# Performance work log

Measured on AMD Instinct MI355X. Metric: run time of the kernel, lower is better.

Reference implementation:

```python
import jax, jax.numpy as jnp
import numpy as np

QUERY_DIM = 1024
CONTEXT_DIM = 1024
HEADS = 8
DIM_HEAD = 64
INNER = HEADS * DIM_HEAD  # 512
SCALE = DIM_HEAD ** -0.5


def setup_inputs() -> dict:
    key = jax.random.key(0)
    ks = jax.random.split(key, 7)
    B, N, M = 2, 2048, 2048
    x = jax.random.normal(ks[0], (B, N, QUERY_DIM), dtype=jnp.float32)
    context = jax.random.normal(ks[1], (B, M, CONTEXT_DIM), dtype=jnp.float32)
    # nn.Linear weights (stored as [out, in] in torch; we use [in, out] here)
    Wq = jax.random.normal(ks[2], (QUERY_DIM, INNER), dtype=jnp.float32) * (QUERY_DIM ** -0.5)
    Wk = jax.random.normal(ks[3], (CONTEXT_DIM, INNER), dtype=jnp.float32) * (CONTEXT_DIM ** -0.5)
    Wv = jax.random.normal(ks[4], (CONTEXT_DIM, INNER), dtype=jnp.float32) * (CONTEXT_DIM ** -0.5)
    Wo = jax.random.normal(ks[5], (INNER, QUERY_DIM), dtype=jnp.float32) * (INNER ** -0.5)
    bo = jax.random.normal(ks[6], (QUERY_DIM,), dtype=jnp.float32) * 0.01
    return {"x": x, "context": context, "Wq": Wq, "Wk": Wk, "Wv": Wv, "Wo": Wo, "bo": bo}


def reference(x, context, Wq, Wk, Wv, Wo, bo):
    B, N, _ = x.shape
    M = context.shape[1]
    # projections (no bias, matching nn.Linear(bias=False))
    q = (x @ Wq).reshape(B, N, HEADS, DIM_HEAD)          # b i h d
    k = (context @ Wk).reshape(B, M, HEADS, DIM_HEAD)    # b j h d
    v = (context @ Wv).reshape(B, M, HEADS, DIM_HEAD)    # b j h d
    # scores in fp32 (ATTN_PRECISION=='fp32' path)
    sim = jnp.einsum('bihd,bjhd->bhij', q.astype(jnp.float32), k.astype(jnp.float32)) * SCALE
    attn = jax.nn.softmax(sim, axis=-1).astype(v.dtype)  # b h i j
    out = jnp.einsum('bhij,bjhd->bihd', attn, v).reshape(B, N, INNER)
    return out @ Wo + bo  # dropout p=0.0 is identity
```

## Files before the change

### kernel.cpp

```cpp
#include <hip/hip_runtime.h>
#include <math.h>

typedef __bf16 bf16_t;
typedef __bf16 bf16x8 __attribute__((ext_vector_type(8)));
typedef __bf16 bf16x4 __attribute__((ext_vector_type(4)));
typedef float  f32x4  __attribute__((ext_vector_type(4)));

#define MFMA16(a, b, c) __builtin_amdgcn_mfma_f32_16x16x32_bf16((a), (b), (c), 0, 0, 0)

#define INNER   512
#define DHEAD   64
#define QSCALE  0.18033688f

__device__ __forceinline__ void g2l(const bf16_t* g, bf16_t* l) {
  __builtin_amdgcn_global_load_lds(
      (const __attribute__((address_space(1))) unsigned int*)g,
      (__attribute__((address_space(3))) unsigned int*)l, 16, 0, 0);
}

__global__ __launch_bounds__(256) void pre_k(const float* __restrict__ x,
                                             const float* __restrict__ ctx,
                                             const float* __restrict__ Wq,
                                             const float* __restrict__ Wk,
                                             const float* __restrict__ Wv,
                                             const float* __restrict__ Wo,
                                             bf16_t* __restrict__ xb,
                                             bf16_t* __restrict__ cb,
                                             bf16_t* __restrict__ WqT,
                                             bf16_t* __restrict__ WkT,
                                             bf16_t* __restrict__ WvT,
                                             bf16_t* __restrict__ WoT) {
  __shared__ float tile[64][65];
  int bx = blockIdx.x;
  if (bx < 8192) {
    const float* in = (bx >= 4096) ? ctx : x;
    bf16_t* out     = (bx >= 4096) ? cb  : xb;
    int i = (bx & 4095) * 256 + threadIdx.x;
    float4 f = ((const float4*)in)[i];
    bf16x4 v = { (bf16_t)f.x, (bf16_t)f.y, (bf16_t)f.z, (bf16_t)f.w };
    ((bf16x4*)out)[i] = v;
    return;
  }
  int t = bx - 8192;
  int z = t >> 7, bid = t & 127;
  const float* W; bf16_t* WT; int K, N;
  if (z == 0)      { W = Wq; WT = WqT; K = 1024; N = 512; }
  else if (z == 1) { W = Wk; WT = WkT; K = 1024; N = 512; }
  else if (z == 2) { W = Wv; WT = WvT; K = 1024; N = 512; }
  else             { W = Wo; WT = WoT; K = 512;  N = 1024; }
  int tK = K >> 6;
  int kt = bid % tK, nt = bid / tK;
  int k0 = kt << 6, n0 = nt << 6;
  for (int idx = threadIdx.x; idx < 4096; idx += 256) {
    int r = idx >> 6, c = idx & 63;
    tile[r][c] = W[(size_t)(k0 + r) * N + n0 + c];
  }
  __syncthreads();
  for (int idx = threadIdx.x; idx < 4096; idx += 256) {
    int r = idx >> 6, c = idx & 63;
    WT[(size_t)(n0 + r) * K + k0 + c] = (bf16_t)tile[c][r];
  }
}

__device__ __forceinline__ void gemm128(const bf16_t* __restrict__ A,
                                        const bf16_t* __restrict__ Bt,
                                        int K, int N, int row0, int n0,
                                        int mode, float scale,
                                        bf16_t* __restrict__ Cb,
                                        float* __restrict__ Cf,
                                        const float* __restrict__ bias) {
  __shared__ bf16_t As[2 * 128 * 64];
  __shared__ bf16_t Bs[2 * 128 * 64];
  const int tid = threadIdx.x;
  const int w = tid >> 6, lane = tid & 63, quad = lane >> 4, l16 = lane & 15;

  const int sr8  = lane >> 3;
  const int slog = ((lane & 7) ^ sr8) << 3;
  const bf16_t* ga = A  + (size_t)(row0 + w * 32 + sr8) * K + slog;
  const bf16_t* gb = Bt + (size_t)(n0   + w * 32 + sr8) * K + slog;
  bf16_t* lA = As + w * 2048;
  bf16_t* lB = Bs + w * 2048;

  f32x4 acc[4][4];
#pragma unroll
  for (int i = 0; i < 4; ++i)
#pragma unroll
    for (int j = 0; j < 4; ++j) acc[i][j] = f32x4{0.f, 0.f, 0.f, 0.f};

  const int mrow = (w & 1) << 6, ncol = (w >> 1) << 6;
  const int KT = K >> 6;

#pragma unroll
  for (int p = 0; p < 4; ++p) {
    g2l(ga + (size_t)(p * 8) * K, lA + p * 512);
    g2l(gb + (size_t)(p * 8) * K, lB + p * 512);
  }

  for (int kc = 0; kc < KT; ++kc) {
    const int cur = (kc & 1) * 8192, nxt = ((kc + 1) & 1) * 8192;
    __syncthreads();
    if (kc + 1 < KT) {
      const int k0 = (kc + 1) * 64;
#pragma unroll
      for (int p = 0; p < 4; ++p) {
        g2l(ga + (size_t)(p * 8) * K + k0, lA + nxt + p * 512);
        g2l(gb + (size_t)(p * 8) * K + k0, lB + nxt + p * 512);
      }
    }
#pragma unroll
    for (int ks = 0; ks < 2; ++ks) {
      const int phys = ((ks * 4 + quad) ^ (l16 & 7)) << 3;
      bf16x8 af[4], bfr[4];
#pragma unroll
      for (int i = 0; i < 4; ++i)
        af[i] = *(const bf16x8*)&As[cur + (mrow + i * 16 + l16) * 64 + phys];
#pragma unroll
      for (int j = 0; j < 4; ++j)
        bfr[j] = *(const bf16x8*)&Bs[cur + (ncol + j * 16 + l16) * 64 + phys];
#pragma unroll
      for (int i = 0; i < 4; ++i)
#pragma unroll
        for (int j = 0; j < 4; ++j)
          acc[i][j] = MFMA16(af[i], bfr[j], acc[i][j]);
    }
  }

#pragma unroll
  for (int i = 0; i < 4; ++i) {
    int row = row0 + mrow + i * 16 + quad * 4;
#pragma unroll
    for (int j = 0; j < 4; ++j) {
      int col = n0 + ncol + j * 16 + l16;
      if (mode == 2) {
        int bb = row >> 11, key = row & 2047;
        int hh = col >> 6,  d   = col & 63;
        bf16x4 v = { (bf16_t)acc[i][j][0], (bf16_t)acc[i][j][1],
                     (bf16_t)acc[i][j][2], (bf16_t)acc[i][j][3] };
        *(bf16x4*)&Cb[((size_t)((bb * 8 + hh) * 64 + d)) * 2048 + key] = v;
      } else {
#pragma unroll
        for (int r = 0; r < 4; ++r) {
          if (mode == 1) Cf[(size_t)(row + r) * N + col] = acc[i][j][r] + bias[col];
          else           Cb[(size_t)(row + r) * N + col] = (bf16_t)(acc[i][j][r] * scale);
        }
      }
    }
  }
}

__global__ __launch_bounds__(256, 2) void gemm_qkv_k(const bf16_t* __restrict__ xb,
                                                     const bf16_t* __restrict__ cb,
                                                     const bf16_t* __restrict__ WqT,
                                                     const bf16_t* __restrict__ WkT,
                                                     const bf16_t* __restrict__ WvT,
                                                     bf16_t* __restrict__ Qb,
                                                     bf16_t* __restrict__ Kb,
                                                     bf16_t* __restrict__ Vt) {
  int z = blockIdx.z;
  const bf16_t* A  = (z == 0) ? xb  : cb;
  const bf16_t* Bt = (z == 0) ? WqT : (z == 1) ? WkT : WvT;
  bf16_t* C        = (z == 0) ? Qb  : (z == 1) ? Kb  : Vt;
  int mode         = (z == 2) ? 2 : 0;
  float scale      = (z == 0) ? QSCALE : 1.0f;
  gemm128(A, Bt, 1024, 512, blockIdx.y * 128, blockIdx.x * 128, mode, scale,
          C, nullptr, nullptr);
}

__global__ __launch_bounds__(256, 2) void gemm_out_k(const bf16_t* __restrict__ AO,
                                                     const bf16_t* __restrict__ WoT,
                                                     const float* __restrict__ bo,
                                                     float* __restrict__ out) {
  gemm128(AO, WoT, 512, 1024, blockIdx.y * 128, blockIdx.x * 128, 1, 1.0f,
          nullptr, out, bo);
}

__global__ __launch_bounds__(256, 2) void attn_k(const bf16_t* __restrict__ Qb,
                                                 const bf16_t* __restrict__ Kb,
                                                 const bf16_t* __restrict__ Vt,
                                                 bf16_t* __restrict__ AO) {
  const int tid = threadIdx.x;
  const int w = tid >> 6, lane = tid & 63, quad = lane >> 4, l16 = lane & 15;
  const int qt = blockIdx.x;
  const int bh = blockIdx.y;
  const int b = bh >> 3, h = bh & 7;

  __shared__ bf16_t Ks[2 * 128 * 64];
  __shared__ bf16_t Vs[64 * 128];
  __shared__ bf16_t Ps[64 * 136];

  const int qrow = b * 2048 + qt * 64 + w * 16 + l16;
  const bf16_t* qptr = Qb + (size_t)qrow * INNER + h * DHEAD;
  bf16x8 bq[2];
  bq[0] = *(const bf16x8*)(qptr + quad * 8);
  bq[1] = *(const bf16x8*)(qptr + 32 + quad * 8);

  f32x4 o[4];
#pragma unroll
  for (int dt = 0; dt < 4; ++dt) o[dt] = f32x4{0.f, 0.f, 0.f, 0.f};
  float m_s = -__builtin_inff(), l_s = 0.f;

  const bf16_t* kbase  = Kb + ((size_t)b * 2048) * INNER + h * DHEAD;
  const bf16_t* vtbase = Vt + ((size_t)bh * 64) * 2048;

  const int krow = lane >> 3;
  const int kcol = ((lane & 7) ^ (lane >> 3)) << 3;
  const int vrow = lane >> 4;

#pragma unroll
  for (int p = 0; p < 4; ++p)
    g2l(kbase + (size_t)(w * 32 + p * 8 + krow) * INNER + kcol,
        &Ks[w * 2048 + p * 512]);

  for (int kt = 0; kt < 16; ++kt) {
    const int cur = (kt & 1) * 8192, nxt = ((kt + 1) & 1) * 8192;
    __syncthreads();
    if (kt < 16 - 1) {
#pragma unroll
      for (int p = 0; p < 4; ++p)
        g2l(kbase + (size_t)((kt + 1) * 128 + w * 32 + p * 8 + krow) * INNER + kcol,
            &Ks[nxt + w * 2048 + p * 512]);
    }
#pragma unroll
    for (int p = 0; p < 4; ++p) {
      int vlog = ((lane & 15) ^ ((p * 4 + vrow) & 15)) << 3;
      g2l(vtbase + (size_t)(w * 16 + p * 4 + vrow) * 2048 + kt * 128 + vlog,
          &Vs[w * 2048 + p * 512]);
    }

    f32x4 s[8];
#pragma unroll
    for (int jt = 0; jt < 8; ++jt) s[jt] = f32x4{0.f, 0.f, 0.f, 0.f};
#pragma unroll
    for (int jt = 0; jt < 8; ++jt) {
#pragma unroll
      for (int ks = 0; ks < 2; ++ks) {
        int phys = ((ks * 4 + quad) ^ (l16 & 7)) << 3;
        bf16x8 ak = *(const bf16x8*)&Ks[cur + (jt * 16 + l16) * 64 + phys];
        s[jt] = MFMA16(ak, bq[ks], s[jt]);
      }
    }

    float mx = -__builtin_inff();
#pragma unroll
    for (int jt = 0; jt < 8; ++jt) {
      float a = fmaxf(fmaxf(s[jt][0], s[jt][1]), fmaxf(s[jt][2], s[jt][3]));
      mx = fmaxf(mx, a);
    }
    mx = fmaxf(mx, __shfl_xor(mx, 16, 64));
    mx = fmaxf(mx, __shfl_xor(mx, 32, 64));
    float mnew = fmaxf(m_s, mx);
    float alpha = __builtin_amdgcn_exp2f(m_s - mnew);
    float rs = 0.f;
#pragma unroll
    for (int jt = 0; jt < 8; ++jt) {
#pragma unroll
      for (int r = 0; r < 4; ++r) {
        float p = __builtin_amdgcn_exp2f(s[jt][r] - mnew);
        s[jt][r] = p;
        rs += p;
      }
    }
    rs += __shfl_xor(rs, 16, 64);
    rs += __shfl_xor(rs, 32, 64);
    l_s = l_s * alpha + rs;
    m_s = mnew;
#pragma unroll
    for (int dt = 0; dt < 4; ++dt) o[dt] *= alpha;

#pragma unroll
    for (int jt = 0; jt < 8; ++jt) {
      bf16x4 pk = { (bf16_t)s[jt][0], (bf16_t)s[jt][1],
                    (bf16_t)s[jt][2], (bf16_t)s[jt][3] };
      *(bf16x4*)&Ps[(w * 16 + l16) * 136 + jt * 16 + quad * 4] = pk;
    }

    __syncthreads();

#pragma unroll
    for (int kc = 0; kc < 4; ++kc) {
      bf16x8 bp = *(const bf16x8*)&Ps[(w * 16 + l16) * 136 + kc * 32 + quad * 8];
#pragma unroll
      for (int dt = 0; dt < 4; ++dt) {
        int phys = ((kc * 4 + quad) ^ l16) << 3;
        bf16x8 av = *(const bf16x8*)&Vs[(dt * 16 + l16) * 128 + phys];
        o[dt] = MFMA16(av, bp, o[dt]);
      }
    }
  }

  float inv = 1.0f / l_s;
#pragma unroll
  for (int dt = 0; dt < 4; ++dt) {
    bf16x4 ov = { (bf16_t)(o[dt][0] * inv), (bf16_t)(o[dt][1] * inv),
                  (bf16_t)(o[dt][2] * inv), (bf16_t)(o[dt][3] * inv) };
    *(bf16x4*)&Ps[(w * 16 + l16) * 136 + dt * 16 + quad * 4] = ov;
  }
  __syncthreads();
  {
    int sr = tid >> 2, sc = (tid & 3) << 4;
    int4 r0 = *(const int4*)&Ps[sr * 136 + sc];
    int4 r1 = *(const int4*)&Ps[sr * 136 + sc + 8];
    bf16_t* aout = AO + ((size_t)(b * 2048 + qt * 64 + sr)) * INNER + h * DHEAD + sc;
    *(int4*)aout       = r0;
    *(int4*)(aout + 8) = r1;
  }
}

extern "C" void kernel_launch(void* const* d_in, const int* in_sizes, int n_in,
                              void* d_out, int out_size, void* d_ws, size_t ws_size,
                              hipStream_t stream) {
  const float* x   = (const float*)d_in[0];
  const float* ctx = (const float*)d_in[1];
  const float* Wq  = (const float*)d_in[2];
  const float* Wk  = (const float*)d_in[3];
  const float* Wv  = (const float*)d_in[4];
  const float* Wo  = (const float*)d_in[5];
  const float* bo  = (const float*)d_in[6];
  float* out = (float*)d_out;

  char* ws = (char*)d_ws;
  const size_t MB = 1048576;
  bf16_t* xb  = (bf16_t*)(ws + 0 * MB);
  bf16_t* cb  = (bf16_t*)(ws + 8 * MB);
  bf16_t* WqT = (bf16_t*)(ws + 16 * MB);
  bf16_t* WkT = (bf16_t*)(ws + 17 * MB);
  bf16_t* WvT = (bf16_t*)(ws + 18 * MB);
  bf16_t* WoT = (bf16_t*)(ws + 19 * MB);
  bf16_t* Qb  = (bf16_t*)(ws + 20 * MB);
  bf16_t* Kb  = (bf16_t*)(ws + 24 * MB);
  bf16_t* Vt  = (bf16_t*)(ws + 28 * MB);
  bf16_t* AO  = (bf16_t*)(ws + 32 * MB);

  pre_k<<<8704, 256, 0, stream>>>(x, ctx, Wq, Wk, Wv, Wo, xb, cb, WqT, WkT, WvT, WoT);
  gemm_qkv_k<<<dim3(4, 32, 3), 256, 0, stream>>>(xb, cb, WqT, WkT, WvT, Qb, Kb, Vt);
  attn_k<<<dim3(32, 16), 256, 0, stream>>>(Qb, Kb, Vt, AO);
  gemm_out_k<<<dim3(8, 32), 256, 0, stream>>>(AO, WoT, bo, out);
}
```

Before: 166.9 us.

## Fuse fp32-to-bf16 activation conversion into QKV GEMM and shrink out-GEMM tile

Removes the separate pass that converted x and context to bf16 in workspace. The QKV GEMM now loads fp32 activations straight into registers, converts them, and writes bf16 into shared memory, with the next tile's loads issued before the MFMA loop. This avoids a full write and re-read of 16 MB of bf16 activations. It also halves the output GEMM's M tile to 64 rows, doubling the grid for better CU occupancy, at the cost of less B-tile reuse. The fp32 path uses more registers and doubles global read traffic for A compared with bf16.

After: 169.5 us. Within noise of the previous version (+1.6%).

```diff
diff --git a/kernel.cpp b/kernel.cpp
--- a/kernel.cpp
+++ b/kernel.cpp
@@ -18,30 +18,16 @@
       (__attribute__((address_space(3))) unsigned int*)l, 16, 0, 0);
 }
 
-__global__ __launch_bounds__(256) void pre_k(const float* __restrict__ x,
-                                             const float* __restrict__ ctx,
-                                             const float* __restrict__ Wq,
-                                             const float* __restrict__ Wk,
-                                             const float* __restrict__ Wv,
-                                             const float* __restrict__ Wo,
-                                             bf16_t* __restrict__ xb,
-                                             bf16_t* __restrict__ cb,
-                                             bf16_t* __restrict__ WqT,
-                                             bf16_t* __restrict__ WkT,
-                                             bf16_t* __restrict__ WvT,
-                                             bf16_t* __restrict__ WoT) {
+__global__ __launch_bounds__(256) void pre_w_k(const float* __restrict__ Wq,
+                                               const float* __restrict__ Wk,
+                                               const float* __restrict__ Wv,
+                                               const float* __restrict__ Wo,
+                                               bf16_t* __restrict__ WqT,
+                                               bf16_t* __restrict__ WkT,
+                                               bf16_t* __restrict__ WvT,
+                                               bf16_t* __restrict__ WoT) {
   __shared__ float tile[64][65];
-  int bx = blockIdx.x;
-  if (bx < 8192) {
-    const float* in = (bx >= 4096) ? ctx : x;
-    bf16_t* out     = (bx >= 4096) ? cb  : xb;
-    int i = (bx & 4095) * 256 + threadIdx.x;
-    float4 f = ((const float4*)in)[i];
-    bf16x4 v = { (bf16_t)f.x, (bf16_t)f.y, (bf16_t)f.z, (bf16_t)f.w };
-    ((bf16x4*)out)[i] = v;
-    return;
-  }
-  int t = bx - 8192;
+  int t = blockIdx.x;
   int z = t >> 7, bid = t & 127;
   const float* W; bf16_t* WT; int K, N;
   if (z == 0)      { W = Wq; WT = WqT; K = 1024; N = 512; }
@@ -62,71 +48,120 @@
   }
 }
 
-__device__ __forceinline__ void gemm128(const bf16_t* __restrict__ A,
-                                        const bf16_t* __restrict__ Bt,
-                                        int K, int N, int row0, int n0,
-                                        int mode, float scale,
-                                        bf16_t* __restrict__ Cb,
-                                        float* __restrict__ Cf,
-                                        const float* __restrict__ bias) {
-  __shared__ bf16_t As[2 * 128 * 64];
+template<int BM, bool AF32>
+__device__ __forceinline__ void gemm_core(const void* __restrict__ Ap,
+                                          const bf16_t* __restrict__ Bt,
+                                          int K, int N, int row0, int n0,
+                                          int mode, float scale,
+                                          bf16_t* __restrict__ Cb,
+                                          float* __restrict__ Cf,
+                                          const float* __restrict__ bias) {
+  constexpr int MI = BM / 32;
+  __shared__ bf16_t As[2 * BM * 64];
   __shared__ bf16_t Bs[2 * 128 * 64];
   const int tid = threadIdx.x;
   const int w = tid >> 6, lane = tid & 63, quad = lane >> 4, l16 = lane & 15;
 
   const int sr8  = lane >> 3;
   const int slog = ((lane & 7) ^ sr8) << 3;
-  const bf16_t* ga = A  + (size_t)(row0 + w * 32 + sr8) * K + slog;
-  const bf16_t* gb = Bt + (size_t)(n0   + w * 32 + sr8) * K + slog;
-  bf16_t* lA = As + w * 2048;
+  const float*  gaF = nullptr;
+  const bf16_t* gaB = nullptr;
+  {
+    size_t aoff = (size_t)(row0 + w * (BM / 4) + sr8) * K + slog;
+    if constexpr (AF32) gaF = (const float*)Ap + aoff;
+    else                gaB = (const bf16_t*)Ap + aoff;
+  }
+  const bf16_t* gb = Bt + (size_t)(n0 + w * 32 + sr8) * K + slog;
+  bf16_t* lA = As + w * (BM / 4) * 64;
   bf16_t* lB = Bs + w * 2048;
 
-  f32x4 acc[4][4];
-#pragma unroll
-  for (int i = 0; i < 4; ++i)
+  f32x4 acc[MI][4];
+#pragma unroll
+  for (int i = 0; i < MI; ++i)
 #pragma unroll
     for (int j = 0; j < 4; ++j) acc[i][j] = f32x4{0.f, 0.f, 0.f, 0.f};
 
-  const int mrow = (w & 1) << 6, ncol = (w >> 1) << 6;
+  const int mrow = (w & 1) * (BM / 2), ncol = (w >> 1) << 6;
   const int KT = K >> 6;
 
-#pragma unroll
-  for (int p = 0; p < 4; ++p) {
-    g2l(ga + (size_t)(p * 8) * K, lA + p * 512);
+  if constexpr (AF32) {
+#pragma unroll
+    for (int p = 0; p < MI; ++p) {
+      const float* s = gaF + (size_t)(p * 8) * K;
+      f32x4 f0 = *(const f32x4*)s;
+      f32x4 f1 = *(const f32x4*)(s + 4);
+      bf16x8 h;
+#pragma unroll
+      for (int e = 0; e < 4; ++e) { h[e] = (bf16_t)f0[e]; h[4 + e] = (bf16_t)f1[e]; }
+      *(bf16x8*)&lA[p * 512 + lane * 8] = h;
+    }
+  } else {
+#pragma unroll
+    for (int p = 0; p < MI; ++p)
+      g2l(gaB + (size_t)(p * 8) * K, lA + p * 512);
+  }
+#pragma unroll
+  for (int p = 0; p < 4; ++p)
     g2l(gb + (size_t)(p * 8) * K, lB + p * 512);
-  }
 
   for (int kc = 0; kc < KT; ++kc) {
-    const int cur = (kc & 1) * 8192, nxt = ((kc + 1) & 1) * 8192;
+    const int curA = (kc & 1) * (BM * 64), nxtA = ((kc + 1) & 1) * (BM * 64);
+    const int curB = (kc & 1) * 8192,      nxtB = ((kc + 1) & 1) * 8192;
     __syncthreads();
-    if (kc + 1 < KT) {
+    f32x4 fpre[2 * MI];
+    const bool pf = (kc + 1 < KT);
+    if (pf) {
       const int k0 = (kc + 1) * 64;
 #pragma unroll
-      for (int p = 0; p < 4; ++p) {
-        g2l(ga + (size_t)(p * 8) * K + k0, lA + nxt + p * 512);
-        g2l(gb + (size_t)(p * 8) * K + k0, lB + nxt + p * 512);
+      for (int p = 0; p < 4; ++p)
+        g2l(gb + (size_t)(p * 8) * K + k0, lB + nxtB + p * 512);
+      if constexpr (AF32) {
+#pragma unroll
+        for (int p = 0; p < MI; ++p) {
+          const float* s = gaF + (size_t)(p * 8) * K + k0;
+          fpre[2 * p]     = *(const f32x4*)s;
+          fpre[2 * p + 1] = *(const f32x4*)(s + 4);
+        }
+      } else {
+#pragma unroll
+        for (int p = 0; p < MI; ++p)
+          g2l(gaB + (size_t)(p * 8) * K + k0, lA + nxtA + p * 512);
       }
     }
 #pragma unroll
     for (int ks = 0; ks < 2; ++ks) {
       const int phys = ((ks * 4 + quad) ^ (l16 & 7)) << 3;
-      bf16x8 af[4], bfr[4];
-#pragma unroll
-      for (int i = 0; i < 4; ++i)
-        af[i] = *(const bf16x8*)&As[cur + (mrow + i * 16 + l16) * 64 + phys];
+      bf16x8 af[MI], bfr[4];
+#pragma unroll
+      for (int i = 0; i < MI; ++i)
+        af[i] = *(const bf16x8*)&As[curA + (mrow + i * 16 + l16) * 64 + phys];
 #pragma unroll
       for (int j = 0; j < 4; ++j)
-        bfr[j] = *(const bf16x8*)&Bs[cur + (ncol + j * 16 + l16) * 64 + phys];
-#pragma unroll
-      for (int i = 0; i < 4; ++i)
+        bfr[j] = *(const bf16x8*)&Bs[curB + (ncol + j * 16 + l16) * 64 + phys];
+#pragma unroll
+      for (int i = 0; i < MI; ++i)
 #pragma unroll
         for (int j = 0; j < 4; ++j)
           acc[i][j] = MFMA16(af[i], bfr[j], acc[i][j]);
     }
-  }
-
-#pragma unroll
-  for (int i = 0; i < 4; ++i) {
+    if (pf) {
+      if constexpr (AF32) {
+#pragma unroll
+        for (int p = 0; p < MI; ++p) {
+          bf16x8 h;
+#pragma unroll
+          for (int e = 0; e < 4; ++e) {
+            h[e]     = (bf16_t)fpre[2 * p][e];
+            h[4 + e] = (bf16_t)fpre[2 * p + 1][e];
+          }
+          *(bf16x8*)&lA[nxtA + p * 512 + lane * 8] = h;
+        }
+      }
+    }
+  }
+
+#pragma unroll
+  for (int i = 0; i < MI; ++i) {
     int row = row0 + mrow + i * 16 + quad * 4;
 #pragma unroll
     for (int j = 0; j < 4; ++j) {
@@ -148,8 +183,8 @@
   }
 }
 
-__global__ __launch_bounds__(256, 2) void gemm_qkv_k(const bf16_t* __restrict__ xb,
-                                                     const bf16_t* __restrict__ cb,
+__global__ __launch_bounds__(256, 2) void gemm_qkv_k(const float* __restrict__ x,
+                                                     const float* __restrict__ ctx,
                                                      const bf16_t* __restrict__ WqT,
                                                      const bf16_t* __restrict__ WkT,
                                                      const bf16_t* __restrict__ WvT,
@@ -157,21 +192,21 @@
                                                      bf16_t* __restrict__ Kb,
                                                      bf16_t* __restrict__ Vt) {
   int z = blockIdx.z;
-  const bf16_t* A  = (z == 0) ? xb  : cb;
+  const float* A   = (z == 0) ? x   : ctx;
   const bf16_t* Bt = (z == 0) ? WqT : (z == 1) ? WkT : WvT;
   bf16_t* C        = (z == 0) ? Qb  : (z == 1) ? Kb  : Vt;
   int mode         = (z == 2) ? 2 : 0;
   float scale      = (z == 0) ? QSCALE : 1.0f;
-  gemm128(A, Bt, 1024, 512, blockIdx.y * 128, blockIdx.x * 128, mode, scale,
-          C, nullptr, nullptr);
+  gemm_core<128, true>(A, Bt, 1024, 512, blockIdx.y * 128, blockIdx.x * 128,
+                       mode, scale, C, nullptr, nullptr);
 }
 
 __global__ __launch_bounds__(256, 2) void gemm_out_k(const bf16_t* __restrict__ AO,
                                                      const bf16_t* __restrict__ WoT,
                                                      const float* __restrict__ bo,
                                                      float* __restrict__ out) {
-  gemm128(AO, WoT, 512, 1024, blockIdx.y * 128, blockIdx.x * 128, 1, 1.0f,
-          nullptr, out, bo);
+  gemm_core<64, false>(AO, WoT, 512, 1024, blockIdx.y * 64, blockIdx.x * 128,
+                       1, 1.0f, nullptr, out, bo);
 }
 
 __global__ __launch_bounds__(256, 2) void attn_k(const bf16_t* __restrict__ Qb,
@@ -320,19 +355,17 @@
 
   char* ws = (char*)d_ws;
   const size_t MB = 1048576;
-  bf16_t* xb  = (bf16_t*)(ws + 0 * MB);
-  bf16_t* cb  = (bf16_t*)(ws + 8 * MB);
-  bf16_t* WqT = (bf16_t*)(ws + 16 * MB);
-  bf16_t* WkT = (bf16_t*)(ws + 17 * MB);
-  bf16_t* WvT = (bf16_t*)(ws + 18 * MB);
-  bf16_t* WoT = (bf16_t*)(ws + 19 * MB);
-  bf16_t* Qb  = (bf16_t*)(ws + 20 * MB);
-  bf16_t* Kb  = (bf16_t*)(ws + 24 * MB);
-  bf16_t* Vt  = (bf16_t*)(ws + 28 * MB);
-  bf16_t* AO  = (bf16_t*)(ws + 32 * MB);
-
-  pre_k<<<8704, 256, 0, stream>>>(x, ctx, Wq, Wk, Wv, Wo, xb, cb, WqT, WkT, WvT, WoT);
-  gemm_qkv_k<<<dim3(4, 32, 3), 256, 0, stream>>>(xb, cb, WqT, WkT, WvT, Qb, Kb, Vt);
+  bf16_t* WqT = (bf16_t*)(ws + 0 * MB);
+  bf16_t* WkT = (bf16_t*)(ws + 1 * MB);
+  bf16_t* WvT = (bf16_t*)(ws + 2 * MB);
+  bf16_t* WoT = (bf16_t*)(ws + 3 * MB);
+  bf16_t* Qb  = (bf16_t*)(ws + 4 * MB);
+  bf16_t* Kb  = (bf16_t*)(ws + 8 * MB);
+  bf16_t* Vt  = (bf16_t*)(ws + 12 * MB);
+  bf16_t* AO  = (bf16_t*)(ws + 16 * MB);
+
+  pre_w_k<<<512, 256, 0, stream>>>(Wq, Wk, Wv, Wo, WqT, WkT, WvT, WoT);
+  gemm_qkv_k<<<dim3(4, 32, 3), 256, 0, stream>>>(x, ctx, WqT, WkT, WvT, Qb, Kb, Vt);
   attn_k<<<dim3(32, 16), 256, 0, stream>>>(Qb, Kb, Vt, AO);
-  gemm_out_k<<<dim3(8, 32), 256, 0, stream>>>(AO, WoT, bo, out);
-}
+  gemm_out_k<<<dim3(8, 64), 256, 0, stream>>>(AO, WoT, bo, out);
+}
```
